# Performance work log

Measured on AMD Instinct MI355X. Metric: run time of the kernel, lower is better.

Reference implementation:

```python
import jax, jax.numpy as jnp
import numpy as np

N, H, E, P = 100000, 64, 1600000, 3


def setup_inputs() -> dict:
    key = jax.random.key(0)
    ks = jax.random.split(key, 12)
    h = jax.random.normal(ks[0], (N, H), dtype=jnp.float32)
    W = jax.random.normal(ks[1], (P, H, H), dtype=jnp.float32) * 0.1
    b = jnp.zeros((P, H), dtype=jnp.float32)
    a = jnp.full((P,), 0.25, dtype=jnp.float32)  # PReLU slopes (torch default init)
    fc_w = jax.random.normal(ks[2], (H, H), dtype=jnp.float32) * 0.1
    fc_b = jnp.zeros((H,), dtype=jnp.float32)
    att = jax.random.normal(ks[3], (H,), dtype=jnp.float32) * 0.1
    adj_vals = jax.random.uniform(ks[4], (E,), dtype=jnp.float32) * (1.0 / 16.0)
    row = jax.random.randint(ks[5], (E,), 0, N, dtype=jnp.int32)
    col = jax.random.randint(ks[6], (E,), 0, N, dtype=jnp.int32)
    mask1 = jax.random.randint(ks[7], (N,), 0, 2, dtype=jnp.int32).astype(bool)
    mask2 = jax.random.randint(ks[8], (N,), 0, 2, dtype=jnp.int32).astype(bool)
    return {"h": h, "W": W, "b": b, "a": a, "fc_w": fc_w, "fc_b": fc_b,
            "att": att, "adj_vals": adj_vals, "row": row, "col": col,
            "mask1": mask1, "mask2": mask2}


def reference(h, W, b, a, fc_w, fc_b, att, adj_vals, row, col, mask1, mask2):
    n = h.shape[0]

    def gcn_all(x):
        # P GCN layers (small fixed P): linear -> spmm(adj) -> +bias -> PReLU
        outs = []
        for p in range(W.shape[0]):
            fts = x @ W[p].T                                   # [N,H]
            msg = fts[col] * adj_vals[:, None]                  # [E,H] gather
            agg = jax.ops.segment_sum(msg, row, num_segments=n) # [N,H] scatter-add
            o = agg + b[p]
            outs.append(jnp.where(o > 0, o, a[p] * o))          # PReLU
        return jnp.stack(outs)                                  # [P,N,H]

    def attention(embeds):
        # sp_p = mean_n tanh(fc(embed_p)); beta = softmax_p(att . sp_p)
        s = jnp.tanh(jnp.einsum('pnh,kh->pnk', embeds, fc_w) + fc_b).mean(axis=1)  # [P,H]
        beta = jax.nn.softmax(s @ att, axis=0)                                      # [P]
        return jnp.einsum('pnh,p->nh', embeds, beta)                                # [N,H]

    h_masked = h * (~mask1)[:, None].astype(h.dtype)
    z_mp = attention(gcn_all(h_masked))       # encode with mask_ratio1
    z_mp2 = attention(gcn_all(h))             # encode with mask_ratio 0
    z_masked = z_mp * (~mask2)[:, None].astype(h.dtype)
    x_recon = attention(gcn_all(z_masked))    # decode
    return (z_mp, z_mp2, x_recon)
```

## Files before the change

kernel.cpp:

```cpp
#include <hip/hip_runtime.h>
#include <hip/hip_bf16.h>

typedef __hip_bfloat16 bf16;
typedef __attribute__((ext_vector_type(8))) short bf16x8;
typedef __attribute__((ext_vector_type(4))) float f32x4;


__device__ __forceinline__ short f2bf(float x) {
    unsigned u = __float_as_uint(x);
    unsigned r = (u + 0x7FFFu + ((u >> 16) & 1u)) >> 16;
    return (short)r;
}
__device__ __forceinline__ float bf2f(short s) {
    return __uint_as_float(((unsigned)(unsigned short)s) << 16);
}
__device__ __forceinline__ void split1(float v, short& h, short& l) {
    h = f2bf(v);
    l = f2bf(v - bf2f(h));
}

__device__ __forceinline__ void split8(const float* __restrict__ p, bool ok, bf16x8& hi,
                                       bf16x8& lo) {
    float v[8];
    if (ok) {
        float4 x0 = ((const float4*)p)[0];
        float4 x1 = ((const float4*)p)[1];
        v[0] = x0.x; v[1] = x0.y; v[2] = x0.z; v[3] = x0.w;
        v[4] = x1.x; v[5] = x1.y; v[6] = x1.z; v[7] = x1.w;
    } else {
#pragma unroll
        for (int j = 0; j < 8; j++) v[j] = 0.f;
    }
#pragma unroll
    for (int j = 0; j < 8; j++) {
        short hb = f2bf(v[j]);
        hi[j] = hb;
        lo[j] = f2bf(v[j] - bf2f(hb));
    }
}

__device__ __forceinline__ float fast_tanh(float x) {
    x = fminf(fmaxf(x, -15.f), 15.f);
    float t = __expf(2.f * x);
    return __fdividef(t - 1.f, t + 1.f);
}

__device__ __forceinline__ void fma4(float4& acc, float v, const float4& x) {
    acc.x = fmaf(v, x.x, acc.x);
    acc.y = fmaf(v, x.y, acc.y);
    acc.z = fmaf(v, x.z, acc.z);
    acc.w = fmaf(v, x.w, acc.w);
}

__device__ __forceinline__ void red4(float4& a) {
    a.x += __shfl_xor(a.x, 16); a.y += __shfl_xor(a.y, 16);
    a.z += __shfl_xor(a.z, 16); a.w += __shfl_xor(a.w, 16);
    a.x += __shfl_xor(a.x, 32); a.y += __shfl_xor(a.y, 32);
    a.z += __shfl_xor(a.z, 32); a.w += __shfl_xor(a.w, 32);
}

__global__ __launch_bounds__(256) void forensic_kernel(const unsigned int* __restrict__ mask_w,
                                                       const unsigned int* __restrict__ idx_w,
                                                       int nw_mask, int nw_idx,
                                                       int* __restrict__ flags) {
    __shared__ int sm[6];
    int t = threadIdx.x;
    if (t < 6) sm[t] = 0;
    __syncthreads();
    int m_gt1 = 0, m_f32 = 0, m_f64 = 0, m_oddnz = 0, i_hi = 0, i_oddnz = 0;
    for (int i = t; i < nw_mask; i += 256) {
        unsigned int w = mask_w[i];
        if (w > 1u && w != 0x3F800000u && w != 0x3FF00000u) m_gt1++;
        if (w == 0x3F800000u) m_f32++;
        if ((i & 1) && w == 0x3FF00000u) m_f64++;
        if ((i & 1) && w != 0u) m_oddnz++;
    }
    for (int i = t; i < nw_idx; i += 256) {
        unsigned int v = idx_w[i];
        if (v >= 0x20000000u) i_hi++;
        if ((i & 1) && v != 0u) i_oddnz++;
    }
    atomicAdd(&sm[0], m_gt1);
    atomicAdd(&sm[1], m_f32);
    atomicAdd(&sm[2], m_f64);
    atomicAdd(&sm[3], m_oddnz);
    atomicAdd(&sm[4], i_hi);
    atomicAdd(&sm[5], i_oddnz);
    __syncthreads();
    if (t == 0) {
        int mmode;
        if (sm[1] > 50) mmode = 2;
        else if (sm[2] > 50) mmode = 4;
        else if (sm[0] > 50) mmode = 0;
        else if (sm[3] > 50) mmode = 1;
        else mmode = 3;
        int imode;
        if (sm[4] > (nw_idx * 3) / 4) imode = 2;
        else if (sm[4] > nw_idx / 4) imode = 4;
        else if (sm[5] > 50) imode = 1;
        else imode = 3;
        flags[0] = mmode;
        flags[1] = imode;
    }
}

__device__ __forceinline__ int fetch_idx(const void* p, int e, int mode) {
    switch (mode) {
        case 1: return ((const int*)p)[e];
        case 3: return (int)(((const long long*)p)[e]);
        case 2: return (int)(((const float*)p)[e]);
        default: return (int)(((const double*)p)[e]);
    }
}

__device__ __forceinline__ bool conv_one(const void* m, int mode, int i) {
    switch (mode) {
        case 0: return ((const unsigned char*)m)[i] != 0;
        case 1: return ((const int*)m)[i] != 0;
        case 2: return ((const float*)m)[i] != 0.f;
        case 3: return ((const long long*)m)[i] != 0;
        default: return ((const double*)m)[i] != 0.0;
    }
}

__global__ __launch_bounds__(256) void conv_masks(const void* __restrict__ m1,
                                                  const void* __restrict__ m2,
                                                  const int* __restrict__ flags, int n,
                                                  unsigned char* __restrict__ o1,
                                                  unsigned char* __restrict__ o2) {
    int mode = flags[0];
    int i = blockIdx.x * 256 + threadIdx.x;
    if (i >= n) return;
    o1[i] = conv_one(m1, mode, i) ? 1 : 0;
    o2[i] = conv_one(m2, mode, i) ? 1 : 0;
}


__global__ __launch_bounds__(256) void bucket_hist(const void* __restrict__ row,
                                                   const int* __restrict__ flags, int e_cnt,
                                                   int n, int shift, int nb,
                                                   int* __restrict__ bcnt) {
    __shared__ int hist[2048];
    int t = threadIdx.x;
    for (int i = t; i < nb; i += 256) hist[i] = 0;
    __syncthreads();
    int imode = flags[1];
    for (int e = blockIdx.x * 256 + t; e < e_cnt; e += gridDim.x * 256) {
        int r = fetch_idx(row, e, imode);
        if ((unsigned)r < (unsigned)n) atomicAdd(&hist[r >> shift], 1);
    }
    __syncthreads();
    for (int i = t; i < nb; i += 256)
        if (hist[i]) atomicAdd(&bcnt[i], hist[i]);
}

__global__ __launch_bounds__(1024) void bucket_scan(int* __restrict__ bptr, int nb,
                                                    int* __restrict__ bcur, int n,
                                                    int* __restrict__ row_ptr) {
    __shared__ int sh[1024];
    int t = threadIdx.x;
    int i0 = t * 2, i1 = t * 2 + 1;
    int a = (i0 < nb) ? bptr[i0] : 0;
    int b = (i1 < nb) ? bptr[i1] : 0;
    int s = a + b;
    sh[t] = s;
    __syncthreads();
    for (int off = 1; off < 1024; off <<= 1) {
        int u = (t >= off) ? sh[t - off] : 0;
        __syncthreads();
        sh[t] += u;
        __syncthreads();
    }
    int base = sh[t] - s;
    if (i0 < nb) { bptr[i0] = base; bcur[i0] = base; }
    if (i1 < nb) { bptr[i1] = base + a; bcur[i1] = base + a; }
    if (t == 1023) {
        bptr[nb] = sh[1023];
        row_ptr[n] = sh[1023];
    }
}

__global__ __launch_bounds__(256) void bin_pass2(const void* __restrict__ row,
                                                 const void* __restrict__ col,
                                                 const float* __restrict__ vals,
                                                 const int* __restrict__ flags, int e_cnt, int n,
                                                 int shift, int nb, int* __restrict__ bcur,
                                                 int2* __restrict__ rcbin,
                                                 float* __restrict__ valbin) {
    __shared__ int hist[2048];
    __shared__ int base[2048];
    int t = threadIdx.x;
    int e0 = blockIdx.x * 2048;
    if (e0 >= e_cnt) return;
    int imode = flags[1];
    for (int i = t; i < nb; i += 256) hist[i] = 0;
    __syncthreads();
    int rr[8], cc[8];
    float vv[8];
    bool ok[8];
#pragma unroll
    for (int j = 0; j < 8; j++) {
        int e = e0 + j * 256 + t;
        ok[j] = false;
        if (e < e_cnt) {
            int r = fetch_idx(row, e, imode);
            if ((unsigned)r < (unsigned)n) {
                ok[j] = true;
                rr[j] = r;
                int c = fetch_idx(col, e, imode);
                cc[j] = ((unsigned)c < (unsigned)n) ? c : 0;
                vv[j] = vals[e];
                atomicAdd(&hist[r >> shift], 1);
            }
        }
    }
    __syncthreads();
    for (int i = t; i < nb; i += 256) {
        int c = hist[i];
        base[i] = c ? atomicAdd(&bcur[i], c) : 0;
        hist[i] = 0;
    }
    __syncthreads();
#pragma unroll
    for (int j = 0; j < 8; j++) {
        if (ok[j]) {
            int bk = rr[j] >> shift;
            int pos = base[bk] + atomicAdd(&hist[bk], 1);
            rcbin[pos] = make_int2(rr[j], cc[j]);
            valbin[pos] = vv[j];
        }
    }
}

__global__ __launch_bounds__(512) void csr_finalize(const int* __restrict__ bptr,
                                                    const int2* __restrict__ rcbin,
                                                    const float* __restrict__ valbin, int n,
                                                    int shift, int* __restrict__ row_ptr,
                                                    int* __restrict__ col_s,
                                                    float* __restrict__ val_s) {
    __shared__ int cnt[1024];
    __shared__ int curs[1024];
    __shared__ int red[512];
    int b = blockIdx.x, t = threadIdx.x;
    int rpb = 1 << shift;
    int r0 = b << shift;
    int rows = n - r0;
    if (rows <= 0) return;
    if (rows > rpb) rows = rpb;
    int ebase = bptr[b], eend = bptr[b + 1];
    for (int i = t; i < rows; i += 512) cnt[i] = 0;
    __syncthreads();
    for (int e = ebase + t; e < eend; e += 512) atomicAdd(&cnt[rcbin[e].x - r0], 1);
    __syncthreads();
    int v[2], s = 0;
#pragma unroll
    for (int j = 0; j < 2; j++) {
        int idx = t * 2 + j;
        v[j] = (idx < rows) ? cnt[idx] : 0;
        s += v[j];
    }
    red[t] = s;
    __syncthreads();
    for (int off = 1; off < 512; off <<= 1) {
        int u = (t >= off) ? red[t - off] : 0;
        __syncthreads();
        red[t] += u;
        __syncthreads();
    }
    int run = ebase + red[t] - s;
#pragma unroll
    for (int j = 0; j < 2; j++) {
        int idx = t * 2 + j;
        if (idx < rows) {
            row_ptr[r0 + idx] = run;
            curs[idx] = run;
            run += v[j];
        }
    }
    __syncthreads();
    for (int e = ebase + t; e < eend; e += 512) {
        int2 rc = rcbin[e];
        float vv = valbin[e];
        int pos = atomicAdd(&curs[rc.x - r0], 1);
        col_s[pos] = rc.y;
        val_s[pos] = vv;
    }
}


__global__ __launch_bounds__(256) void spmm_dual(const float* __restrict__ X,
                                                 const int* __restrict__ row_ptr,
                                                 const int* __restrict__ col_s,
                                                 const float* __restrict__ val_s,
                                                 const unsigned char* __restrict__ mask, int n,
                                                 short* __restrict__ axm_hi,
                                                 short* __restrict__ axm_lo,
                                                 short* __restrict__ axf_hi,
                                                 short* __restrict__ axf_lo) {
    int gid = blockIdx.x * 256 + threadIdx.x;
    int r = gid >> 6;
    if (r >= n) return;
    int lane = threadIdx.x & 63;
    int g = lane >> 4, sub = lane & 15;
    int s = row_ptr[r], e = row_ptr[r + 1];
    int cnt = e - s;
    int myc = 0;
    float myvf = 0.f, myvm = 0.f;
    if (lane < cnt) {
        myc = col_s[s + lane];
        float v = val_s[s + lane];
        myvf = v;
        myvm = mask[myc] ? 0.f : v;
    }
    int cmain = cnt > 64 ? 64 : cnt;
    float4 fA = {0, 0, 0, 0}, fB = {0, 0, 0, 0}, mA = {0, 0, 0, 0}, mB = {0, 0, 0, 0};
    for (int i = 0; i < cmain; i += 16) {
        int i0 = i + g, i1 = i + 4 + g, i2 = i + 8 + g, i3 = i + 12 + g;
        int c0 = __shfl(myc, i0), c1 = __shfl(myc, i1);
        int c2 = __shfl(myc, i2), c3 = __shfl(myc, i3);
        float vf0 = __shfl(myvf, i0), vf1 = __shfl(myvf, i1);
        float vf2 = __shfl(myvf, i2), vf3 = __shfl(myvf, i3);
        float vm0 = __shfl(myvm, i0), vm1 = __shfl(myvm, i1);
        float vm2 = __shfl(myvm, i2), vm3 = __shfl(myvm, i3);
        if (i0 < cmain) {
            float4 x = *(const float4*)(X + (size_t)c0 * 64 + sub * 4);
            fma4(fA, vf0, x);
            fma4(mA, vm0, x);
        }
        if (i1 < cmain) {
            float4 x = *(const float4*)(X + (size_t)c1 * 64 + sub * 4);
            fma4(fB, vf1, x);
            fma4(mB, vm1, x);
        }
        if (i2 < cmain) {
            float4 x = *(const float4*)(X + (size_t)c2 * 64 + sub * 4);
            fma4(fA, vf2, x);
            fma4(mA, vm2, x);
        }
        if (i3 < cmain) {
            float4 x = *(const float4*)(X + (size_t)c3 * 64 + sub * 4);
            fma4(fB, vf3, x);
            fma4(mB, vm3, x);
        }
    }
    for (int i = 64 + g; i < cnt; i += 4) {
        int c = col_s[s + i];
        float v = val_s[s + i];
        float vm = mask[c] ? 0.f : v;
        float4 x = *(const float4*)(X + (size_t)c * 64 + sub * 4);
        fma4(fA, v, x);
        fma4(mA, vm, x);
    }
    fA.x += fB.x; fA.y += fB.y; fA.z += fB.z; fA.w += fB.w;
    mA.x += mB.x; mA.y += mB.y; mA.z += mB.z; mA.w += mB.w;
    red4(fA);
    red4(mA);
    if (g == 0) {
        size_t o = (size_t)r * 64 + sub * 4;
        short4 h4, l4;
        split1(fA.x, h4.x, l4.x); split1(fA.y, h4.y, l4.y);
        split1(fA.z, h4.z, l4.z); split1(fA.w, h4.w, l4.w);
        *(short4*)(axf_hi + o) = h4;
        *(short4*)(axf_lo + o) = l4;
        split1(mA.x, h4.x, l4.x); split1(mA.y, h4.y, l4.y);
        split1(mA.z, h4.z, l4.z); split1(mA.w, h4.w, l4.w);
        *(short4*)(axm_hi + o) = h4;
        *(short4*)(axm_lo + o) = l4;
    }
}

__global__ __launch_bounds__(256) void spmm_one(const float* __restrict__ X,
                                                const int* __restrict__ row_ptr,
                                                const int* __restrict__ col_s,
                                                const float* __restrict__ val_s,
                                                const unsigned char* __restrict__ mask, int n,
                                                short* __restrict__ ax_hi,
                                                short* __restrict__ ax_lo) {
    int gid = blockIdx.x * 256 + threadIdx.x;
    int r = gid >> 6;
    if (r >= n) return;
    int lane = threadIdx.x & 63;
    int g = lane >> 4, sub = lane & 15;
    int s = row_ptr[r], e = row_ptr[r + 1];
    int cnt = e - s;
    int myc = 0;
    float myv = 0.f;
    if (lane < cnt) {
        myc = col_s[s + lane];
        float v = val_s[s + lane];
        myv = mask[myc] ? 0.f : v;
    }
    int cmain = cnt > 64 ? 64 : cnt;
    float4 aA = {0, 0, 0, 0}, aB = {0, 0, 0, 0};
    for (int i = 0; i < cmain; i += 16) {
        int i0 = i + g, i1 = i + 4 + g, i2 = i + 8 + g, i3 = i + 12 + g;
        int c0 = __shfl(myc, i0), c1 = __shfl(myc, i1);
        int c2 = __shfl(myc, i2), c3 = __shfl(myc, i3);
        float v0 = __shfl(myv, i0), v1 = __shfl(myv, i1);
        float v2 = __shfl(myv, i2), v3 = __shfl(myv, i3);
        if (i0 < cmain && v0 != 0.f) {
            float4 x = *(const float4*)(X + (size_t)c0 * 64 + sub * 4);
            fma4(aA, v0, x);
        }
        if (i1 < cmain && v1 != 0.f) {
            float4 x = *(const float4*)(X + (size_t)c1 * 64 + sub * 4);
            fma4(aB, v1, x);
        }
        if (i2 < cmain && v2 != 0.f) {
            float4 x = *(const float4*)(X + (size_t)c2 * 64 + sub * 4);
            fma4(aA, v2, x);
        }
        if (i3 < cmain && v3 != 0.f) {
            float4 x = *(const float4*)(X + (size_t)c3 * 64 + sub * 4);
            fma4(aB, v3, x);
        }
    }
    for (int i = 64 + g; i < cnt; i += 4) {
        int c = col_s[s + i];
        if (mask[c]) continue;
        float v = val_s[s + i];
        float4 x = *(const float4*)(X + (size_t)c * 64 + sub * 4);
        fma4(aA, v, x);
    }
    aA.x += aB.x; aA.y += aB.y; aA.z += aB.z; aA.w += aB.w;
    red4(aA);
    if (g == 0) {
        size_t o = (size_t)r * 64 + sub * 4;
        short4 h4, l4;
        split1(aA.x, h4.x, l4.x); split1(aA.y, h4.y, l4.y);
        split1(aA.z, h4.z, l4.z); split1(aA.w, h4.w, l4.w);
        *(short4*)(ax_hi + o) = h4;
        *(short4*)(ax_lo + o) = l4;
    }
}


template <int PP>
__global__ __launch_bounds__(256) void gemm_tanh(const short* __restrict__ Xhi,
                                                 const short* __restrict__ Xlo,
                                                 const float* __restrict__ Wg,
                                                 const float* __restrict__ b,
                                                 const float* __restrict__ a,
                                                 const float* __restrict__ fcw,
                                                 const float* __restrict__ fcb, int n, int ntiles,
                                                 float* __restrict__ s_sums) {
    __shared__ __align__(16) short ehi[PP][16][72], elo[PP][16][72];
    int t = threadIdx.x;
    int wv = t >> 6, lane = t & 63, nl = lane & 15, q = lane >> 4;
    int colg = wv * 16 + nl;
    bf16x8 whi[PP][2], wlo[PP][2];
    float bias[PP], slope[PP];
#pragma unroll
    for (int p = 0; p < PP; p++) {
#pragma unroll
        for (int kk = 0; kk < 2; kk++)
            split8(Wg + p * 4096 + colg * 64 + kk * 32 + q * 8, true, whi[p][kk], wlo[p][kk]);
        bias[p] = b[p * 64 + colg];
        slope[p] = a[p];
    }
    bf16x8 fhi[2], flo[2];
#pragma unroll
    for (int kk = 0; kk < 2; kk++)
        split8(fcw + colg * 64 + kk * 32 + q * 8, true, fhi[kk], flo[kk]);
    float fbias = fcb[colg];
    float ssum[PP];
#pragma unroll
    for (int p = 0; p < PP; p++) ssum[p] = 0.f;

    int rt = blockIdx.x;
    bf16x8 ah[2], al[2];
    if (rt < ntiles) {
        size_t rb = (size_t)(rt * 16 + nl) * 64 + q * 8;
#pragma unroll
        for (int kk = 0; kk < 2; kk++) {
            ah[kk] = *(const bf16x8*)(Xhi + rb + kk * 32);
            al[kk] = *(const bf16x8*)(Xlo + rb + kk * 32);
        }
    }
    for (; rt < ntiles; rt += gridDim.x) {
#pragma unroll
        for (int p = 0; p < PP; p++) {
            f32x4 acc = {0.f, 0.f, 0.f, 0.f};
            acc = __builtin_amdgcn_mfma_f32_16x16x32_bf16(ah[0], whi[p][0], acc, 0, 0, 0);
            acc = __builtin_amdgcn_mfma_f32_16x16x32_bf16(ah[1], whi[p][1], acc, 0, 0, 0);
            acc = __builtin_amdgcn_mfma_f32_16x16x32_bf16(al[0], whi[p][0], acc, 0, 0, 0);
            acc = __builtin_amdgcn_mfma_f32_16x16x32_bf16(al[1], whi[p][1], acc, 0, 0, 0);
            acc = __builtin_amdgcn_mfma_f32_16x16x32_bf16(ah[0], wlo[p][0], acc, 0, 0, 0);
            acc = __builtin_amdgcn_mfma_f32_16x16x32_bf16(ah[1], wlo[p][1], acc, 0, 0, 0);
            acc = __builtin_amdgcn_mfma_f32_16x16x32_bf16(al[0], wlo[p][0], acc, 0, 0, 0);
            acc = __builtin_amdgcn_mfma_f32_16x16x32_bf16(al[1], wlo[p][1], acc, 0, 0, 0);
#pragma unroll
            for (int i = 0; i < 4; i++) {
                float o = acc[i] + bias[p];
                o = (o > 0.f) ? o : slope[p] * o;
                short hb, lb;
                split1(o, hb, lb);
                ehi[p][q * 4 + i][colg] = hb;
                elo[p][q * 4 + i][colg] = lb;
            }
        }
        int rn = rt + gridDim.x;
        bf16x8 pfh[2], pfl[2];
        if (rn < ntiles) {
            size_t rb = (size_t)(rn * 16 + nl) * 64 + q * 8;
#pragma unroll
            for (int kk = 0; kk < 2; kk++) {
                pfh[kk] = *(const bf16x8*)(Xhi + rb + kk * 32);
                pfl[kk] = *(const bf16x8*)(Xlo + rb + kk * 32);
            }
        }
        __syncthreads();
#pragma unroll
        for (int p = 0; p < PP; p++) {
            bf16x8 eh[2], el[2];
#pragma unroll
            for (int kk = 0; kk < 2; kk++) {
                eh[kk] = *(const bf16x8*)(&ehi[p][nl][kk * 32 + q * 8]);
                el[kk] = *(const bf16x8*)(&elo[p][nl][kk * 32 + q * 8]);
            }
            f32x4 acc = {0.f, 0.f, 0.f, 0.f};
            acc = __builtin_amdgcn_mfma_f32_16x16x32_bf16(eh[0], fhi[0], acc, 0, 0, 0);
            acc = __builtin_amdgcn_mfma_f32_16x16x32_bf16(eh[1], fhi[1], acc, 0, 0, 0);
            acc = __builtin_amdgcn_mfma_f32_16x16x32_bf16(el[0], fhi[0], acc, 0, 0, 0);
            acc = __builtin_amdgcn_mfma_f32_16x16x32_bf16(el[1], fhi[1], acc, 0, 0, 0);
            acc = __builtin_amdgcn_mfma_f32_16x16x32_bf16(eh[0], flo[0], acc, 0, 0, 0);
            acc = __builtin_amdgcn_mfma_f32_16x16x32_bf16(eh[1], flo[1], acc, 0, 0, 0);
#pragma unroll
            for (int i = 0; i < 4; i++) {
                int r = rt * 16 + q * 4 + i;
                if (r < n) ssum[p] += fast_tanh(acc[i] + fbias);
            }
        }
        __syncthreads();
#pragma unroll
        for (int kk = 0; kk < 2; kk++) {
            ah[kk] = pfh[kk];
            al[kk] = pfl[kk];
        }
    }
#pragma unroll
    for (int p = 0; p < PP; p++) {
        float s = ssum[p];
        s += __shfl_xor(s, 16);
        s += __shfl_xor(s, 32);
        if (q == 0) atomicAdd(&s_sums[p * 64 + colg], s);
    }
}


template <int PP>
__global__ __launch_bounds__(256) void gemm_mix(const short* __restrict__ Xhi,
                                                const short* __restrict__ Xlo,
                                                const float* __restrict__ Wg,
                                                const float* __restrict__ b,
                                                const float* __restrict__ a,
                                                const float* __restrict__ beta, int n, int ntiles,
                                                float* __restrict__ out, int accum) {
    int t = threadIdx.x;
    int wv = t >> 6, lane = t & 63, nl = lane & 15, q = lane >> 4;
    int colg = wv * 16 + nl;
    bf16x8 whi[PP][2], wlo[PP][2];
    float bias[PP], slope[PP], bet[PP];
#pragma unroll
    for (int p = 0; p < PP; p++) {
#pragma unroll
        for (int kk = 0; kk < 2; kk++)
            split8(Wg + p * 4096 + colg * 64 + kk * 32 + q * 8, true, whi[p][kk], wlo[p][kk]);
        bias[p] = b[p * 64 + colg];
        slope[p] = a[p];
        bet[p] = beta[p];
    }
    int rt = blockIdx.x;
    bf16x8 ah[2], al[2];
    if (rt < ntiles) {
        size_t rb = (size_t)(rt * 16 + nl) * 64 + q * 8;
#pragma unroll
        for (int kk = 0; kk < 2; kk++) {
            ah[kk] = *(const bf16x8*)(Xhi + rb + kk * 32);
            al[kk] = *(const bf16x8*)(Xlo + rb + kk * 32);
        }
    }
    for (; rt < ntiles; rt += gridDim.x) {
        int rn = rt + gridDim.x;
        bf16x8 pfh[2], pfl[2];
        if (rn < ntiles) {
            size_t rb = (size_t)(rn * 16 + nl) * 64 + q * 8;
#pragma unroll
            for (int kk = 0; kk < 2; kk++) {
                pfh[kk] = *(const bf16x8*)(Xhi + rb + kk * 32);
                pfl[kk] = *(const bf16x8*)(Xlo + rb + kk * 32);
            }
        }
        float mix[4] = {0.f, 0.f, 0.f, 0.f};
#pragma unroll
        for (int p = 0; p < PP; p++) {
            f32x4 acc = {0.f, 0.f, 0.f, 0.f};
            acc = __builtin_amdgcn_mfma_f32_16x16x32_bf16(ah[0], whi[p][0], acc, 0, 0, 0);
            acc = __builtin_amdgcn_mfma_f32_16x16x32_bf16(ah[1], whi[p][1], acc, 0, 0, 0);
            acc = __builtin_amdgcn_mfma_f32_16x16x32_bf16(al[0], whi[p][0], acc, 0, 0, 0);
            acc = __builtin_amdgcn_mfma_f32_16x16x32_bf16(al[1], whi[p][1], acc, 0, 0, 0);
            acc = __builtin_amdgcn_mfma_f32_16x16x32_bf16(ah[0], wlo[p][0], acc, 0, 0, 0);
            acc = __builtin_amdgcn_mfma_f32_16x16x32_bf16(ah[1], wlo[p][1], acc, 0, 0, 0);
            acc = __builtin_amdgcn_mfma_f32_16x16x32_bf16(al[0], wlo[p][0], acc, 0, 0, 0);
            acc = __builtin_amdgcn_mfma_f32_16x16x32_bf16(al[1], wlo[p][1], acc, 0, 0, 0);
#pragma unroll
            for (int i = 0; i < 4; i++) {
                float o = acc[i] + bias[p];
                o = (o > 0.f) ? o : slope[p] * o;
                mix[i] = fmaf(bet[p], o, mix[i]);
            }
        }
#pragma unroll
        for (int i = 0; i < 4; i++) {
            int r = rt * 16 + q * 4 + i;
            if (r < n) {
                size_t idx = (size_t)r * 64 + colg;
                out[idx] = accum ? (out[idx] + mix[i]) : mix[i];
            }
        }
#pragma unroll
        for (int kk = 0; kk < 2; kk++) {
            ah[kk] = pfh[kk];
            al[kk] = pfl[kk];
        }
    }
}

__global__ __launch_bounds__(64) void compute_beta(const float* __restrict__ s_sums,
                                                   const float* __restrict__ att, int n, int P,
                                                   float* __restrict__ beta) {
    int lane = threadIdx.x;
    float av = att[lane];
    float l[8];
    for (int p = 0; p < P; p++) l[p] = s_sums[p * 64 + lane] * av;
#pragma unroll
    for (int off = 32; off > 0; off >>= 1)
        for (int p = 0; p < 8; p++)
            if (p < P) l[p] += __shfl_down(l[p], off);
    if (lane == 0) {
        const float inv = 1.0f / (float)n;
        float m = -1e30f;
        for (int p = 0; p < P; p++) {
            l[p] *= inv;
            m = fmaxf(m, l[p]);
        }
        float s = 0.f;
        for (int p = 0; p < P; p++) {
            l[p] = __expf(l[p] - m);
            s += l[p];
        }
        for (int p = 0; p < P; p++) beta[p] = l[p] / s;
    }
}


extern "C" void kernel_launch(void* const* d_in, const int* in_sizes, int n_in,
                              void* d_out, int out_size, void* d_ws, size_t ws_size,
                              hipStream_t stream) {
    const float* h = (const float*)d_in[0];
    const float* W = (const float*)d_in[1];
    const float* b = (const float*)d_in[2];
    const float* a = (const float*)d_in[3];
    const float* fc_w = (const float*)d_in[4];
    const float* fc_b = (const float*)d_in[5];
    const float* att = (const float*)d_in[6];
    const float* adj = (const float*)d_in[7];
    const void* row = d_in[8];
    const void* col = d_in[9];
    const void* mask1 = d_in[10];
    const void* mask2 = d_in[11];
    float* out = (float*)d_out;

    int P = in_sizes[3];
    if (P < 1 || P > 8) P = 3;
    int N = in_sizes[0] / 64;
    int E = in_sizes[7];
    int N16 = (N + 15) & ~15;
    int ntiles = N16 >> 4;

    int shift = 8;
    while (((N >> shift) + 1) > 2048) shift++;
    int NB = (N >> shift) + 1;

    char* w = (char*)d_ws;
    auto alloc = [&](size_t bytes) {
        void* p = (void*)w;
        w += (bytes + 255) & ~(size_t)255;
        return p;
    };
    int* row_ptr = (int*)alloc((size_t)(N + 1) * 4);
    int* col_s = (int*)alloc((size_t)E * 4);
    float* val_s = (float*)alloc((size_t)E * 4);
    int* bptr = (int*)alloc((size_t)(NB + 1) * 4);
    int* bcur = (int*)alloc((size_t)NB * 4);
    int2* rcbin = (int2*)alloc((size_t)E * 8);
    float* valbin = (float*)alloc((size_t)E * 4);
    unsigned char* m1c = (unsigned char*)alloc(N);
    unsigned char* m2c = (unsigned char*)alloc(N);
    short* axm_hi = (short*)alloc((size_t)N16 * 64 * 2);
    short* axm_lo = (short*)alloc((size_t)N16 * 64 * 2);
    short* axf_hi = (short*)alloc((size_t)N16 * 64 * 2);
    short* axf_lo = (short*)alloc((size_t)N16 * 64 * 2);
    float* s_sums = (float*)alloc(8 * 64 * 4);
    float* beta = (float*)alloc(8 * 4);
    int* flags = (int*)alloc(256);

    int nw_mask = N / 4 > 25000 ? 25000 : N / 4;
    int nw_idx = E / 4 > 25000 ? 25000 : E / 4;
    forensic_kernel<<<1, 256, 0, stream>>>((const unsigned int*)mask1, (const unsigned int*)row,
                                           nw_mask, nw_idx, flags);
    conv_masks<<<(N + 255) / 256, 256, 0, stream>>>(mask1, mask2, flags, N, m1c, m2c);

    hipMemsetAsync(bptr, 0, (size_t)(NB + 1) * 4, stream);
    if (N16 > N) {
        size_t padoff = (size_t)N * 64, padbytes = (size_t)(N16 - N) * 64 * 2;
        hipMemsetAsync(axm_hi + padoff, 0, padbytes, stream);
        hipMemsetAsync(axm_lo + padoff, 0, padbytes, stream);
        hipMemsetAsync(axf_hi + padoff, 0, padbytes, stream);
        hipMemsetAsync(axf_lo + padoff, 0, padbytes, stream);
    }
    bucket_hist<<<1024, 256, 0, stream>>>(row, flags, E, N, shift, NB, bptr);
    bucket_scan<<<1, 1024, 0, stream>>>(bptr, NB, bcur, N, row_ptr);
    int bin_blocks = (E + 2047) / 2048;
    bin_pass2<<<bin_blocks, 256, 0, stream>>>(row, col, adj, flags, E, N, shift, NB, bcur, rcbin,
                                              valbin);
    csr_finalize<<<NB, 512, 0, stream>>>(bptr, rcbin, valbin, N, shift, row_ptr, col_s, val_s);

    int spmm_grid = ((size_t)N * 64 + 255) / 256;
    int tanh_blocks = 1024;
    int mix_blocks = 1024;

    auto tail = [&](const short* axhi, const short* axlo, float* dst) {
        hipMemsetAsync(s_sums, 0, 8 * 64 * 4, stream);
        if (P == 3) {
            gemm_tanh<3><<<tanh_blocks, 256, 0, stream>>>(axhi, axlo, W, b, a, fc_w, fc_b, N,
                                                          ntiles, s_sums);
        } else {
            for (int p = 0; p < P; p++)
                gemm_tanh<1><<<tanh_blocks, 256, 0, stream>>>(axhi, axlo, W + p * 4096,
                                                              b + p * 64, a + p, fc_w, fc_b, N,
                                                              ntiles, s_sums + p * 64);
        }
        compute_beta<<<1, 64, 0, stream>>>(s_sums, att, N, P, beta);
        if (P == 3) {
            gemm_mix<3><<<mix_blocks, 256, 0, stream>>>(axhi, axlo, W, b, a, beta, N, ntiles, dst,
                                                        0);
        } else {
            for (int p = 0; p < P; p++)
                gemm_mix<1><<<mix_blocks, 256, 0, stream>>>(axhi, axlo, W + p * 4096, b + p * 64,
                                                            a + p, beta + p, N, ntiles, dst,
                                                            p != 0);
        }
    };

    spmm_dual<<<spmm_grid, 256, 0, stream>>>(h, row_ptr, col_s, val_s, m1c, N, axm_hi, axm_lo,
                                             axf_hi, axf_lo);
    tail(axm_hi, axm_lo, out);
    tail(axf_hi, axf_lo, out + (size_t)N * 64);
    spmm_one<<<spmm_grid, 256, 0, stream>>>(out, row_ptr, col_s, val_s, m2c, N, axm_hi, axm_lo);
    tail(axm_hi, axm_lo, out + (size_t)2 * N * 64);
}
```

Before: 591.2 us.

## Process two rows per wave in SpMM and batch the two encoder tails

```diff
diff --git a/kernel.cpp b/kernel.cpp
--- a/kernel.cpp
+++ b/kernel.cpp
@@ -288,6 +288,15 @@
 }
 
 
+__device__ __forceinline__ void store_split4(short* __restrict__ hi, short* __restrict__ lo,
+                                             size_t o, const float4& v) {
+    short4 h4, l4;
+    split1(v.x, h4.x, l4.x); split1(v.y, h4.y, l4.y);
+    split1(v.z, h4.z, l4.z); split1(v.w, h4.w, l4.w);
+    *(short4*)(hi + o) = h4;
+    *(short4*)(lo + o) = l4;
+}
+
 __global__ __launch_bounds__(256) void spmm_dual(const float* __restrict__ X,
                                                  const int* __restrict__ row_ptr,
                                                  const int* __restrict__ col_s,
@@ -298,75 +307,96 @@
                                                  short* __restrict__ axf_hi,
                                                  short* __restrict__ axf_lo) {
     int gid = blockIdx.x * 256 + threadIdx.x;
-    int r = gid >> 6;
-    if (r >= n) return;
+    int wv = gid >> 6;
+    int r0 = wv * 2;
+    if (r0 >= n) return;
     int lane = threadIdx.x & 63;
     int g = lane >> 4, sub = lane & 15;
-    int s = row_ptr[r], e = row_ptr[r + 1];
-    int cnt = e - s;
-    int myc = 0;
-    float myvf = 0.f, myvm = 0.f;
-    if (lane < cnt) {
-        myc = col_s[s + lane];
-        float v = val_s[s + lane];
-        myvf = v;
-        myvm = mask[myc] ? 0.f : v;
-    }
-    int cmain = cnt > 64 ? 64 : cnt;
-    float4 fA = {0, 0, 0, 0}, fB = {0, 0, 0, 0}, mA = {0, 0, 0, 0}, mB = {0, 0, 0, 0};
-    for (int i = 0; i < cmain; i += 16) {
-        int i0 = i + g, i1 = i + 4 + g, i2 = i + 8 + g, i3 = i + 12 + g;
-        int c0 = __shfl(myc, i0), c1 = __shfl(myc, i1);
-        int c2 = __shfl(myc, i2), c3 = __shfl(myc, i3);
-        float vf0 = __shfl(myvf, i0), vf1 = __shfl(myvf, i1);
-        float vf2 = __shfl(myvf, i2), vf3 = __shfl(myvf, i3);
-        float vm0 = __shfl(myvm, i0), vm1 = __shfl(myvm, i1);
-        float vm2 = __shfl(myvm, i2), vm3 = __shfl(myvm, i3);
-        if (i0 < cmain) {
-            float4 x = *(const float4*)(X + (size_t)c0 * 64 + sub * 4);
-            fma4(fA, vf0, x);
-            fma4(mA, vm0, x);
-        }
-        if (i1 < cmain) {
-            float4 x = *(const float4*)(X + (size_t)c1 * 64 + sub * 4);
-            fma4(fB, vf1, x);
-            fma4(mB, vm1, x);
-        }
-        if (i2 < cmain) {
-            float4 x = *(const float4*)(X + (size_t)c2 * 64 + sub * 4);
-            fma4(fA, vf2, x);
-            fma4(mA, vm2, x);
-        }
-        if (i3 < cmain) {
-            float4 x = *(const float4*)(X + (size_t)c3 * 64 + sub * 4);
-            fma4(fB, vf3, x);
-            fma4(mB, vm3, x);
-        }
-    }
-    for (int i = 64 + g; i < cnt; i += 4) {
-        int c = col_s[s + i];
-        float v = val_s[s + i];
+    int r1 = r0 + 1;
+    bool has1 = r1 < n;
+    int s0 = row_ptr[r0];
+    int e0 = row_ptr[r0 + 1];
+    int e1 = has1 ? row_ptr[r0 + 2] : e0;
+    int s1 = e0;
+    int cnt0 = e0 - s0, cnt1 = e1 - s1;
+    int myc0 = 0, myc1 = 0;
+    float myf0 = 0.f, mym0 = 0.f, myf1 = 0.f, mym1 = 0.f;
+    if (lane < cnt0) {
+        myc0 = col_s[s0 + lane];
+        float v = val_s[s0 + lane];
+        myf0 = v;
+        mym0 = mask[myc0] ? 0.f : v;
+    }
+    if (lane < cnt1) {
+        myc1 = col_s[s1 + lane];
+        float v = val_s[s1 + lane];
+        myf1 = v;
+        mym1 = mask[myc1] ? 0.f : v;
+    }
+    int cm0 = cnt0 > 64 ? 64 : cnt0;
+    int cm1 = cnt1 > 64 ? 64 : cnt1;
+    int cm = cm0 > cm1 ? cm0 : cm1;
+    float4 f0a = {0, 0, 0, 0}, f0b = {0, 0, 0, 0}, m0a = {0, 0, 0, 0}, m0b = {0, 0, 0, 0};
+    float4 f1a = {0, 0, 0, 0}, f1b = {0, 0, 0, 0}, m1a = {0, 0, 0, 0}, m1b = {0, 0, 0, 0};
+    for (int i = 0; i < cm; i += 8) {
+        int iA = i + g, iB = i + 4 + g;
+        int cA0 = __shfl(myc0, iA), cB0 = __shfl(myc0, iB);
+        float fA0 = __shfl(myf0, iA), fB0 = __shfl(myf0, iB);
+        float mA0 = __shfl(mym0, iA), mB0 = __shfl(mym0, iB);
+        int cA1 = __shfl(myc1, iA), cB1 = __shfl(myc1, iB);
+        float fA1 = __shfl(myf1, iA), fB1 = __shfl(myf1, iB);
+        float mA1 = __shfl(mym1, iA), mB1 = __shfl(mym1, iB);
+        if (iA < cm0) {
+            float4 x = *(const float4*)(X + (size_t)cA0 * 64 + sub * 4);
+            fma4(f0a, fA0, x);
+            fma4(m0a, mA0, x);
+        }
+        if (iA < cm1) {
+            float4 x = *(const float4*)(X + (size_t)cA1 * 64 + sub * 4);
+            fma4(f1a, fA1, x);
+            fma4(m1a, mA1, x);
+        }
+        if (iB < cm0) {
+            float4 x = *(const float4*)(X + (size_t)cB0 * 64 + sub * 4);
+            fma4(f0b, fB0, x);
+            fma4(m0b, mB0, x);
+        }
+        if (iB < cm1) {
+            float4 x = *(const float4*)(X + (size_t)cB1 * 64 + sub * 4);
+            fma4(f1b, fB1, x);
+            fma4(m1b, mB1, x);
+        }
+    }
+    for (int i = 64 + g; i < cnt0; i += 4) {
+        int c = col_s[s0 + i];
+        float v = val_s[s0 + i];
         float vm = mask[c] ? 0.f : v;
         float4 x = *(const float4*)(X + (size_t)c * 64 + sub * 4);
-        fma4(fA, v, x);
-        fma4(mA, vm, x);
-    }
-    fA.x += fB.x; fA.y += fB.y; fA.z += fB.z; fA.w += fB.w;
-    mA.x += mB.x; mA.y += mB.y; mA.z += mB.z; mA.w += mB.w;
-    red4(fA);
-    red4(mA);
-    if (g == 0) {
-        size_t o = (size_t)r * 64 + sub * 4;
-        short4 h4, l4;
-        split1(fA.x, h4.x, l4.x); split1(fA.y, h4.y, l4.y);
-        split1(fA.z, h4.z, l4.z); split1(fA.w, h4.w, l4.w);
-        *(short4*)(axf_hi + o) = h4;
-        *(short4*)(axf_lo + o) = l4;
-        split1(mA.x, h4.x, l4.x); split1(mA.y, h4.y, l4.y);
-        split1(mA.z, h4.z, l4.z); split1(mA.w, h4.w, l4.w);
-        *(short4*)(axm_hi + o) = h4;
-        *(short4*)(axm_lo + o) = l4;
-    }
+        fma4(f0a, v, x);
+        fma4(m0a, vm, x);
+    }
+    for (int i = 64 + g; i < cnt1; i += 4) {
+        int c = col_s[s1 + i];
+        float v = val_s[s1 + i];
+        float vm = mask[c] ? 0.f : v;
+        float4 x = *(const float4*)(X + (size_t)c * 64 + sub * 4);
+        fma4(f1a, v, x);
+        fma4(m1a, vm, x);
+    }
+    f0a.x += f0b.x; f0a.y += f0b.y; f0a.z += f0b.z; f0a.w += f0b.w;
+    m0a.x += m0b.x; m0a.y += m0b.y; m0a.z += m0b.z; m0a.w += m0b.w;
+    f1a.x += f1b.x; f1a.y += f1b.y; f1a.z += f1b.z; f1a.w += f1b.w;
+    m1a.x += m1b.x; m1a.y += m1b.y; m1a.z += m1b.z; m1a.w += m1b.w;
+    red4(f0a);
+    red4(m0a);
+    red4(f1a);
+    red4(m1a);
+    size_t o0 = (size_t)r0 * 64 + sub * 4;
+    size_t o1 = (size_t)r1 * 64 + sub * 4;
+    if (g == 0) store_split4(axf_hi, axf_lo, o0, f0a);
+    else if (g == 1) store_split4(axm_hi, axm_lo, o0, m0a);
+    else if (g == 2 && has1) store_split4(axf_hi, axf_lo, o1, f1a);
+    else if (g == 3 && has1) store_split4(axm_hi, axm_lo, o1, m1a);
 }
 
 __global__ __launch_bounds__(256) void spmm_one(const float* __restrict__ X,
@@ -377,67 +407,88 @@
                                                 short* __restrict__ ax_hi,
                                                 short* __restrict__ ax_lo) {
     int gid = blockIdx.x * 256 + threadIdx.x;
-    int r = gid >> 6;
-    if (r >= n) return;
+    int wv = gid >> 6;
+    int r0 = wv * 2;
+    if (r0 >= n) return;
     int lane = threadIdx.x & 63;
     int g = lane >> 4, sub = lane & 15;
-    int s = row_ptr[r], e = row_ptr[r + 1];
-    int cnt = e - s;
-    int myc = 0;
-    float myv = 0.f;
-    if (lane < cnt) {
-        myc = col_s[s + lane];
-        float v = val_s[s + lane];
-        myv = mask[myc] ? 0.f : v;
-    }
-    int cmain = cnt > 64 ? 64 : cnt;
-    float4 aA = {0, 0, 0, 0}, aB = {0, 0, 0, 0};
-    for (int i = 0; i < cmain; i += 16) {
-        int i0 = i + g, i1 = i + 4 + g, i2 = i + 8 + g, i3 = i + 12 + g;
-        int c0 = __shfl(myc, i0), c1 = __shfl(myc, i1);
-        int c2 = __shfl(myc, i2), c3 = __shfl(myc, i3);
-        float v0 = __shfl(myv, i0), v1 = __shfl(myv, i1);
-        float v2 = __shfl(myv, i2), v3 = __shfl(myv, i3);
-        if (i0 < cmain && v0 != 0.f) {
-            float4 x = *(const float4*)(X + (size_t)c0 * 64 + sub * 4);
-            fma4(aA, v0, x);
-        }
-        if (i1 < cmain && v1 != 0.f) {
-            float4 x = *(const float4*)(X + (size_t)c1 * 64 + sub * 4);
-            fma4(aB, v1, x);
-        }
-        if (i2 < cmain && v2 != 0.f) {
-            float4 x = *(const float4*)(X + (size_t)c2 * 64 + sub * 4);
-            fma4(aA, v2, x);
-        }
-        if (i3 < cmain && v3 != 0.f) {
-            float4 x = *(const float4*)(X + (size_t)c3 * 64 + sub * 4);
-            fma4(aB, v3, x);
-        }
-    }
-    for (int i = 64 + g; i < cnt; i += 4) {
-        int c = col_s[s + i];
+    int r1 = r0 + 1;
+    bool has1 = r1 < n;
+    int s0 = row_ptr[r0];
+    int e0 = row_ptr[r0 + 1];
+    int e1 = has1 ? row_ptr[r0 + 2] : e0;
+    int s1 = e0;
+    int cnt0 = e0 - s0, cnt1 = e1 - s1;
+    int myc0 = 0, myc1 = 0;
+    float myv0 = 0.f, myv1 = 0.f;
+    if (lane < cnt0) {
+        myc0 = col_s[s0 + lane];
+        float v = val_s[s0 + lane];
+        myv0 = mask[myc0] ? 0.f : v;
+    }
+    if (lane < cnt1) {
+        myc1 = col_s[s1 + lane];
+        float v = val_s[s1 + lane];
+        myv1 = mask[myc1] ? 0.f : v;
+    }
+    int cm0 = cnt0 > 64 ? 64 : cnt0;
+    int cm1 = cnt1 > 64 ? 64 : cnt1;
+    int cm = cm0 > cm1 ? cm0 : cm1;
+    float4 a0a = {0, 0, 0, 0}, a0b = {0, 0, 0, 0};
+    float4 a1a = {0, 0, 0, 0}, a1b = {0, 0, 0, 0};
+    for (int i = 0; i < cm; i += 8) {
+        int iA = i + g, iB = i + 4 + g;
+        int cA0 = __shfl(myc0, iA), cB0 = __shfl(myc0, iB);
+        float vA0 = __shfl(myv0, iA), vB0 = __shfl(myv0, iB);
+        int cA1 = __shfl(myc1, iA), cB1 = __shfl(myc1, iB);
+        float vA1 = __shfl(myv1, iA), vB1 = __shfl(myv1, iB);
+        if (iA < cm0 && vA0 != 0.f) {
+            float4 x = *(const float4*)(X + (size_t)cA0 * 64 + sub * 4);
+            fma4(a0a, vA0, x);
+        }
+        if (iA < cm1 && vA1 != 0.f) {
+            float4 x = *(const float4*)(X + (size_t)cA1 * 64 + sub * 4);
+            fma4(a1a, vA1, x);
+        }
+        if (iB < cm0 && vB0 != 0.f) {
+            float4 x = *(const float4*)(X + (size_t)cB0 * 64 + sub * 4);
+            fma4(a0b, vB0, x);
+        }
+        if (iB < cm1 && vB1 != 0.f) {
+            float4 x = *(const float4*)(X + (size_t)cB1 * 64 + sub * 4);
+            fma4(a1b, vB1, x);
+        }
+    }
+    for (int i = 64 + g; i < cnt0; i += 4) {
+        int c = col_s[s0 + i];
         if (mask[c]) continue;
-        float v = val_s[s + i];
+        float v = val_s[s0 + i];
         float4 x = *(const float4*)(X + (size_t)c * 64 + sub * 4);
-        fma4(aA, v, x);
-    }
-    aA.x += aB.x; aA.y += aB.y; aA.z += aB.z; aA.w += aB.w;
-    red4(aA);
-    if (g == 0) {
-        size_t o = (size_t)r * 64 + sub * 4;
-        short4 h4, l4;
-        split1(aA.x, h4.x, l4.x); split1(aA.y, h4.y, l4.y);
-        split1(aA.z, h4.z, l4.z); split1(aA.w, h4.w, l4.w);
-        *(short4*)(ax_hi + o) = h4;
-        *(short4*)(ax_lo + o) = l4;
-    }
+        fma4(a0a, v, x);
+    }
+    for (int i = 64 + g; i < cnt1; i += 4) {
+        int c = col_s[s1 + i];
+        if (mask[c]) continue;
+        float v = val_s[s1 + i];
+        float4 x = *(const float4*)(X + (size_t)c * 64 + sub * 4);
+        fma4(a1a, v, x);
+    }
+    a0a.x += a0b.x; a0a.y += a0b.y; a0a.z += a0b.z; a0a.w += a0b.w;
+    a1a.x += a1b.x; a1a.y += a1b.y; a1a.z += a1b.z; a1a.w += a1b.w;
+    red4(a0a);
+    red4(a1a);
+    size_t o0 = (size_t)r0 * 64 + sub * 4;
+    size_t o1 = (size_t)r1 * 64 + sub * 4;
+    if (g == 0) store_split4(ax_hi, ax_lo, o0, a0a);
+    else if (g == 1 && has1) store_split4(ax_hi, ax_lo, o1, a1a);
 }
 
 
 template <int PP>
-__global__ __launch_bounds__(256) void gemm_tanh(const short* __restrict__ Xhi,
-                                                 const short* __restrict__ Xlo,
+__global__ __launch_bounds__(256) void gemm_tanh(const short* __restrict__ Xhi0,
+                                                 const short* __restrict__ Xlo0,
+                                                 const short* __restrict__ Xhi1,
+                                                 const short* __restrict__ Xlo1,
                                                  const float* __restrict__ Wg,
                                                  const float* __restrict__ b,
                                                  const float* __restrict__ a,
@@ -445,6 +496,10 @@
                                                  const float* __restrict__ fcb, int n, int ntiles,
                                                  float* __restrict__ s_sums) {
     __shared__ __align__(16) short ehi[PP][16][72], elo[PP][16][72];
+    int set = blockIdx.y;
+    const short* __restrict__ Xhi = set ? Xhi1 : Xhi0;
+    const short* __restrict__ Xlo = set ? Xlo1 : Xlo0;
+    float* __restrict__ ss = s_sums + set * 512;
     int t = threadIdx.x;
     int wv = t >> 6, lane = t & 63, nl = lane & 15, q = lane >> 4;
     int colg = wv * 16 + nl;
@@ -543,19 +598,25 @@
         float s = ssum[p];
         s += __shfl_xor(s, 16);
         s += __shfl_xor(s, 32);
-        if (q == 0) atomicAdd(&s_sums[p * 64 + colg], s);
+        if (q == 0) atomicAdd(&ss[p * 64 + colg], s);
     }
 }
 
 
 template <int PP>
-__global__ __launch_bounds__(256) void gemm_mix(const short* __restrict__ Xhi,
-                                                const short* __restrict__ Xlo,
+__global__ __launch_bounds__(256) void gemm_mix(const short* __restrict__ Xhi0,
+                                                const short* __restrict__ Xlo0,
+                                                const short* __restrict__ Xhi1,
+                                                const short* __restrict__ Xlo1,
                                                 const float* __restrict__ Wg,
                                                 const float* __restrict__ b,
                                                 const float* __restrict__ a,
                                                 const float* __restrict__ beta, int n, int ntiles,
-                                                float* __restrict__ out, int accum) {
+                                                float* __restrict__ outbase, int accum) {
+    int set = blockIdx.y;
+    const short* __restrict__ Xhi = set ? Xhi1 : Xhi0;
+    const short* __restrict__ Xlo = set ? Xlo1 : Xlo0;
+    float* __restrict__ out = outbase + (size_t)set * n * 64;
     int t = threadIdx.x;
     int wv = t >> 6, lane = t & 63, nl = lane & 15, q = lane >> 4;
     int colg = wv * 16 + nl;
@@ -568,7 +629,7 @@
             split8(Wg + p * 4096 + colg * 64 + kk * 32 + q * 8, true, whi[p][kk], wlo[p][kk]);
         bias[p] = b[p * 64 + colg];
         slope[p] = a[p];
-        bet[p] = beta[p];
+        bet[p] = beta[set * 8 + p];
     }
     int rt = blockIdx.x;
     bf16x8 ah[2], al[2];
@@ -628,28 +689,31 @@
 
 __global__ __launch_bounds__(64) void compute_beta(const float* __restrict__ s_sums,
                                                    const float* __restrict__ att, int n, int P,
-                                                   float* __restrict__ beta) {
+                                                   int nsets, float* __restrict__ beta) {
     int lane = threadIdx.x;
     float av = att[lane];
-    float l[8];
-    for (int p = 0; p < P; p++) l[p] = s_sums[p * 64 + lane] * av;
-#pragma unroll
-    for (int off = 32; off > 0; off >>= 1)
-        for (int p = 0; p < 8; p++)
-            if (p < P) l[p] += __shfl_down(l[p], off);
-    if (lane == 0) {
-        const float inv = 1.0f / (float)n;
-        float m = -1e30f;
-        for (int p = 0; p < P; p++) {
-            l[p] *= inv;
-            m = fmaxf(m, l[p]);
-        }
-        float s = 0.f;
-        for (int p = 0; p < P; p++) {
-            l[p] = __expf(l[p] - m);
-            s += l[p];
-        }
-        for (int p = 0; p < P; p++) beta[p] = l[p] / s;
+    for (int st = 0; st < nsets; st++) {
+        const float* ss = s_sums + st * 512;
+        float l[8];
+        for (int p = 0; p < P; p++) l[p] = ss[p * 64 + lane] * av;
+#pragma unroll
+        for (int off = 32; off > 0; off >>= 1)
+            for (int p = 0; p < 8; p++)
+                if (p < P) l[p] += __shfl_down(l[p], off);
+        if (lane == 0) {
+            const float inv = 1.0f / (float)n;
+            float m = -1e30f;
+            for (int p = 0; p < P; p++) {
+                l[p] *= inv;
+                m = fmaxf(m, l[p]);
+            }
+            float s = 0.f;
+            for (int p = 0; p < P; p++) {
+                l[p] = __expf(l[p] - m);
+                s += l[p];
+            }
+            for (int p = 0; p < P; p++) beta[st * 8 + p] = l[p] / s;
+        }
     }
 }
 
@@ -701,8 +765,8 @@
     short* axm_lo = (short*)alloc((size_t)N16 * 64 * 2);
     short* axf_hi = (short*)alloc((size_t)N16 * 64 * 2);
     short* axf_lo = (short*)alloc((size_t)N16 * 64 * 2);
-    float* s_sums = (float*)alloc(8 * 64 * 4);
-    float* beta = (float*)alloc(8 * 4);
+    float* s_sums = (float*)alloc(2 * 512 * 4);
+    float* beta = (float*)alloc(64 * 4);
     int* flags = (int*)alloc(256);
 
     int nw_mask = N / 4 > 25000 ? 25000 : N / 4;
@@ -726,37 +790,37 @@
                                               valbin);
     csr_finalize<<<NB, 512, 0, stream>>>(bptr, rcbin, valbin, N, shift, row_ptr, col_s, val_s);
 
-    int spmm_grid = ((size_t)N * 64 + 255) / 256;
+    int spmm_grid = (int)(((size_t)((N + 1) / 2) * 64 + 255) / 256);
     int tanh_blocks = 1024;
     int mix_blocks = 1024;
 
-    auto tail = [&](const short* axhi, const short* axlo, float* dst) {
-        hipMemsetAsync(s_sums, 0, 8 * 64 * 4, stream);
+    auto tail = [&](const short* xh0, const short* xl0, const short* xh1, const short* xl1,
+                    int nsets, float* dst) {
+        hipMemsetAsync(s_sums, 0, 2 * 512 * 4, stream);
         if (P == 3) {
-            gemm_tanh<3><<<tanh_blocks, 256, 0, stream>>>(axhi, axlo, W, b, a, fc_w, fc_b, N,
-                                                          ntiles, s_sums);
+            gemm_tanh<3><<<dim3(tanh_blocks, nsets), 256, 0, stream>>>(
+                xh0, xl0, xh1, xl1, W, b, a, fc_w, fc_b, N, ntiles, s_sums);
         } else {
             for (int p = 0; p < P; p++)
-                gemm_tanh<1><<<tanh_blocks, 256, 0, stream>>>(axhi, axlo, W + p * 4096,
-                                                              b + p * 64, a + p, fc_w, fc_b, N,
-                                                              ntiles, s_sums + p * 64);
-        }
-        compute_beta<<<1, 64, 0, stream>>>(s_sums, att, N, P, beta);
+                gemm_tanh<1><<<dim3(tanh_blocks, nsets), 256, 0, stream>>>(
+                    xh0, xl0, xh1, xl1, W + p * 4096, b + p * 64, a + p, fc_w, fc_b, N, ntiles,
+                    s_sums + p * 64);
+        }
+        compute_beta<<<1, 64, 0, stream>>>(s_sums, att, N, P, nsets, beta);
         if (P == 3) {
-            gemm_mix<3><<<mix_blocks, 256, 0, stream>>>(axhi, axlo, W, b, a, beta, N, ntiles, dst,
-                                                        0);
+            gemm_mix<3><<<dim3(mix_blocks, nsets), 256, 0, stream>>>(
+                xh0, xl0, xh1, xl1, W, b, a, beta, N, ntiles, dst, 0);
         } else {
             for (int p = 0; p < P; p++)
-                gemm_mix<1><<<mix_blocks, 256, 0, stream>>>(axhi, axlo, W + p * 4096, b + p * 64,
-                                                            a + p, beta + p, N, ntiles, dst,
-                                                            p != 0);
+                gemm_mix<1><<<dim3(mix_blocks, nsets), 256, 0, stream>>>(
+                    xh0, xl0, xh1, xl1, W + p * 4096, b + p * 64, a + p, beta + p, N, ntiles, dst,
+                    p != 0);
         }
     };
 
     spmm_dual<<<spmm_grid, 256, 0, stream>>>(h, row_ptr, col_s, val_s, m1c, N, axm_hi, axm_lo,
                                              axf_hi, axf_lo);
-    tail(axm_hi, axm_lo, out);
-    tail(axf_hi, axf_lo, out + (size_t)N * 64);
+    tail(axm_hi, axm_lo, axf_hi, axf_lo, 2, out);
     spmm_one<<<spmm_grid, 256, 0, stream>>>(out, row_ptr, col_s, val_s, m2c, N, axm_hi, axm_lo);
-    tail(axm_hi, axm_lo, out + (size_t)2 * N * 64);
-}
+    tail(axm_hi, axm_lo, axm_hi, axm_lo, 1, out + (size_t)2 * N * 64);
+}
```

New measurement: 564.0 us. 1.05x faster.
